# Performance work log

Hardware: AMD Instinct MI355X
Metric: run time of the kernel (lower is better)

## Reference

```python
import jax, jax.numpy as jnp
import numpy as np

EPS = 1e-5  # BatchNorm eps (PyTorch default)


def gcn_conv(x, edge_index, W, b):
    """PyG GCNConv with add_self_loops=True, normalize=True.
    out[j] = sum_{(i->j)} x_w[i] / sqrt(deg_i * deg_j) + x_w[j] / deg_j + b,
    deg_j = 1 + in-degree(j) (self-loop included)."""
    n = x.shape[0]
    src, dst = edge_index[0], edge_index[1]
    ones = jnp.ones(src.shape[0], x.dtype)
    deg = 1.0 + jax.ops.segment_sum(ones, dst, num_segments=n)  # [n]
    dis = jax.lax.rsqrt(deg)
    xw = x @ W  # [n, out]
    msg = xw[src] * (dis[src] * dis[dst])[:, None]  # gather + per-edge norm
    agg = jax.ops.segment_sum(msg, dst, num_segments=n)  # scatter-add
    agg = agg + xw * (1.0 / deg)[:, None]  # self-loop term
    return agg + b


def bn_relu(x, gamma, beta):
    # BatchNorm1d over the node dim (training-mode batch stats) + ReLU
    mean = x.mean(axis=0)
    var = x.var(axis=0)
    return jax.nn.relu((x - mean) * jax.lax.rsqrt(var + EPS) * gamma + beta)


def wireframe_gnn(x, edge_index, layers, fcW, fcb):
    feats = [x]
    h = x
    for (W, b, g, be) in layers:  # fixed small n_layers loop
        h = bn_relu(gcn_conv(h, edge_index, W, b), g, be)
        feats.append(h)
    cat = jnp.concatenate(feats, axis=1)
    return jax.nn.relu(cat @ fcW + fcb)


N_L, N_J = 50000, 25000
D_FC, NF = 1024, 256
E_L, E_J = 400000, 100000
L_LAB, J_LAB = 10, 3


def setup_inputs() -> dict:
    key = jax.random.key(0)
    ks = iter(jax.random.split(key, 48))
    p = lambda shape: (jax.random.normal(next(ks), shape, jnp.float32) * 0.02)
    inp = {}
    inp["line_features"] = jax.random.normal(next(ks), (N_L, D_FC), jnp.float32)
    inp["junction_features"] = jax.random.normal(next(ks), (N_J, NF), jnp.float32)
    inp["line_edge_index"] = jax.random.randint(next(ks), (2, E_L), 0, N_L, jnp.int64)
    inp["junction_edge_index"] = jax.random.randint(next(ks), (2, E_J), 0, N_J, jnp.int64)
    # line GNN: 1024 -> 512 -> 256, concat 1792 -> fc 1024
    inp["lg_W1"], inp["lg_b1"] = p((D_FC, D_FC // 2)), p((D_FC // 2,))
    inp["lg_g1"], inp["lg_be1"] = jnp.ones(D_FC // 2, jnp.float32), jnp.zeros(D_FC // 2, jnp.float32)
    inp["lg_W2"], inp["lg_b2"] = p((D_FC // 2, D_FC // 4)), p((D_FC // 4,))
    inp["lg_g2"], inp["lg_be2"] = jnp.ones(D_FC // 4, jnp.float32), jnp.zeros(D_FC // 4, jnp.float32)
    cat_l = D_FC + D_FC // 2 + D_FC // 4  # 1792
    inp["lg_fcW"], inp["lg_fcb"] = p((cat_l, D_FC)), p((D_FC,))
    # fc_lines: 1024 -> 1024 -> 1024 -> L_LAB (dim_loi*n_pts1 == dim_fc == 1024)
    inp["fl_W1"], inp["fl_b1"] = p((D_FC, D_FC)), p((D_FC,))
    inp["fl_W2"], inp["fl_b2"] = p((D_FC, D_FC)), p((D_FC,))
    inp["fl_W3"], inp["fl_b3"] = p((D_FC, L_LAB)), p((L_LAB,))
    # junction GNN: 256 -> 128 -> 64, concat 448 -> fc 256
    inp["jg_W1"], inp["jg_b1"] = p((NF, NF // 2)), p((NF // 2,))
    inp["jg_g1"], inp["jg_be1"] = jnp.ones(NF // 2, jnp.float32), jnp.zeros(NF // 2, jnp.float32)
    inp["jg_W2"], inp["jg_b2"] = p((NF // 2, NF // 4)), p((NF // 4,))
    inp["jg_g2"], inp["jg_be2"] = jnp.ones(NF // 4, jnp.float32), jnp.zeros(NF // 4, jnp.float32)
    cat_j = NF + NF // 2 + NF // 4  # 448
    inp["jg_fcW"], inp["jg_fcb"] = p((cat_j, NF)), p((NF,))
    # fc_junction: 256 -> 64 -> J_LAB
    m = NF // 4
    inp["fj_W1"], inp["fj_b1"] = p((NF, m)), p((m,))
    inp["fj_W2"], inp["fj_b2"] = p((m, J_LAB)), p((J_LAB,))
    return inp


def reference(line_features, junction_features, line_edge_index, junction_edge_index,
              lg_W1, lg_b1, lg_g1, lg_be1, lg_W2, lg_b2, lg_g2, lg_be2, lg_fcW, lg_fcb,
              fl_W1, fl_b1, fl_W2, fl_b2, fl_W3, fl_b3,
              jg_W1, jg_b1, jg_g1, jg_be1, jg_W2, jg_b2, jg_g2, jg_be2, jg_fcW, jg_fcb,
              fj_W1, fj_b1, fj_W2, fj_b2):
    # line branch
    h = wireframe_gnn(line_features, line_edge_index,
                      [(lg_W1, lg_b1, lg_g1, lg_be1), (lg_W2, lg_b2, lg_g2, lg_be2)],
                      lg_fcW, lg_fcb)
    h = jax.nn.relu(h @ fl_W1 + fl_b1)
    h = jax.nn.relu(h @ fl_W2 + fl_b2)
    line_logits = h @ fl_W3 + fl_b3
    # junction branch
    g = wireframe_gnn(junction_features, junction_edge_index,
                      [(jg_W1, jg_b1, jg_g1, jg_be1), (jg_W2, jg_b2, jg_g2, jg_be2)],
                      jg_fcW, jg_fcb)
    g = jax.nn.relu(g @ fj_W1 + fj_b1)
    junction_logits = g @ fj_W2 + fj_b2
    return (line_logits, junction_logits)
```

## Files before the change

### kernel.cpp

```cpp
#include <hip/hip_runtime.h>
#include <stdint.h>
#include <stddef.h>

typedef _Float16 f16;
typedef _Float16 f16x8 __attribute__((ext_vector_type(8)));
typedef _Float16 f16x4_t __attribute__((ext_vector_type(4)));
typedef float floatx4 __attribute__((ext_vector_type(4)));

template <int N> struct F16Vec { typedef f16 type __attribute__((ext_vector_type(N))); };

#define BN_EPS 1e-5f

struct WtJob { const float* W; f16* Wt; int K; int N; int tN; int tilebase; };
struct WtBatch { WtJob j[12]; int njobs; int ntiles; };

__global__ void k_wt_tiled(WtBatch b) {
  __shared__ float T[32][33];
  int bt = blockIdx.x;
  int i = 0;
  #pragma unroll 1
  while (i + 1 < b.njobs && bt >= b.j[i + 1].tilebase) ++i;
  WtJob J = b.j[i];
  int t = bt - J.tilebase;
  int tr = t / J.tN, tc = t - tr * J.tN;
  int ty = threadIdx.x >> 5, tx = threadIdx.x & 31;
  #pragma unroll
  for (int s = 0; s < 32; s += 8) {
    int k = tr * 32 + ty + s, n = tc * 32 + tx;
    if (k < J.K && n < J.N) T[ty + s][tx] = J.W[(size_t)k * J.N + n];
  }
  __syncthreads();
  #pragma unroll
  for (int s = 0; s < 32; s += 8) {
    int n = tc * 32 + ty + s, k = tr * 32 + tx;
    if (n < J.N && k < J.K) J.Wt[(size_t)n * J.K + k] = (f16)T[tx][ty + s];
  }
}

__global__ void k_cvt_cols(const float* __restrict__ src, f16* __restrict__ dst,
                           int n, int c, int ldd, int coff) {
  int t = blockIdx.x * blockDim.x + threadIdx.x;
  int cq = c >> 2;
  if (t >= n * cq) return;
  int r = t / cq, j = (t - r * cq) << 2;
  float4 v = *(const float4*)(src + (size_t)r * c + j);
  f16x4_t o; o[0] = (f16)v.x; o[1] = (f16)v.y; o[2] = (f16)v.z; o[3] = (f16)v.w;
  *(f16x4_t*)(dst + (size_t)r * ldd + coff + j) = o;
}

__global__ void k_count2(const int* __restrict__ dL, int EL, int* __restrict__ cntL,
                         const int* __restrict__ dJ, int EJ, int* __restrict__ cntJ) {
  int t = blockIdx.x * blockDim.x + threadIdx.x;
  if (t < EL) atomicAdd(&cntL[dL[t]], 1);
  else if (t < EL + EJ) atomicAdd(&cntJ[dJ[t - EL]], 1);
}

__global__ void k_scan4(const int* __restrict__ cnt, int n, int* __restrict__ rowstart,
                        float* __restrict__ dis) {
  __shared__ int wsum[16];
  __shared__ int carry_s;
  int tid = threadIdx.x, lane = tid & 63, wv = tid >> 6;
  if (tid == 0) { carry_s = 0; rowstart[0] = 0; }
  __syncthreads();
  for (int base = 0; base < n; base += 4096) {
    int i4 = base + tid * 4;
    int4 c = {0, 0, 0, 0};
    if (i4 < n) c = *(const int4*)(cnt + i4);
    int s0 = c.x, s1 = s0 + c.y, s2 = s1 + c.z, s3 = s2 + c.w;
    int x = s3;
    #pragma unroll
    for (int off = 1; off < 64; off <<= 1) {
      int y = __shfl_up(x, off, 64);
      if (lane >= off) x += y;
    }
    if (lane == 63) wsum[wv] = x;
    __syncthreads();
    if (wv == 0) {
      int s = (lane < 16) ? wsum[lane] : 0;
      #pragma unroll
      for (int off = 1; off < 16; off <<= 1) {
        int y = __shfl_up(s, off, 64);
        if (lane >= off) s += y;
      }
      if (lane < 16) wsum[lane] = s;
    }
    __syncthreads();
    int waveoff = (wv == 0) ? 0 : wsum[wv - 1];
    int excl = (x - s3) + waveoff + carry_s;
    if (i4 < n) {
      rowstart[i4 + 1] = excl + s0;
      rowstart[i4 + 2] = excl + s1;
      rowstart[i4 + 3] = excl + s2;
      rowstart[i4 + 4] = excl + s3;
      dis[i4 + 0] = rsqrtf(1.0f + (float)c.x);
      dis[i4 + 1] = rsqrtf(1.0f + (float)c.y);
      dis[i4 + 2] = rsqrtf(1.0f + (float)c.z);
      dis[i4 + 3] = rsqrtf(1.0f + (float)c.w);
    }
    __syncthreads();
    if (tid == 1023) carry_s = excl + s3;
    __syncthreads();
  }
}

__global__ void k_fill2(const int* __restrict__ eiL, int EL, const int* __restrict__ rsL,
                        int* __restrict__ fillL, int* __restrict__ cixL,
                        const int* __restrict__ eiJ, int EJ, const int* __restrict__ rsJ,
                        int* __restrict__ fillJ, int* __restrict__ cixJ) {
  int t = blockIdx.x * blockDim.x + threadIdx.x;
  if (t < EL) {
    int s = eiL[t], d = eiL[EL + t];
    int pos = atomicAdd(&fillL[d], 1);
    cixL[rsL[d] + pos] = s;
  } else if (t < EL + EJ) {
    int u = t - EL;
    int s = eiJ[u], d = eiJ[EJ + u];
    int pos = atomicAdd(&fillJ[d], 1);
    cixJ[rsJ[d] + pos] = s;
  }
}

template <int CPL>
__global__ void k_gather_f16(const f16* __restrict__ xw, int C,
                             const int* __restrict__ rowstart, const int* __restrict__ colidx,
                             const float* __restrict__ dis, const float* __restrict__ bias,
                             f16* __restrict__ dst, int ldd, int coff, int n) {
  typedef typename F16Vec<CPL>::type V;
  int w = threadIdx.x >> 6, l = threadIdx.x & 63;
  int j = blockIdx.x * 4 + w;
  if (j >= n) return;
  float dj = dis[j];
  int rs = rowstart[j], re = rowstart[j + 1];
  int c0 = l * CPL;
  float acc[CPL];
  {
    V p = *(const V*)(xw + (size_t)j * C + c0);
    float s = dj * dj;
    #pragma unroll
    for (int t = 0; t < CPL; ++t) acc[t] = (float)p[t] * s;
  }
  int e = rs;
  for (; e + 2 <= re; e += 2) {
    int s0 = colidx[e], s1 = colidx[e + 1];
    float f0 = dis[s0] * dj, f1 = dis[s1] * dj;
    V p0 = *(const V*)(xw + (size_t)s0 * C + c0);
    V p1 = *(const V*)(xw + (size_t)s1 * C + c0);
    #pragma unroll
    for (int t = 0; t < CPL; ++t) acc[t] += (float)p0[t] * f0 + (float)p1[t] * f1;
  }
  if (e < re) {
    int s0 = colidx[e];
    float f0 = dis[s0] * dj;
    V p0 = *(const V*)(xw + (size_t)s0 * C + c0);
    #pragma unroll
    for (int t = 0; t < CPL; ++t) acc[t] += (float)p0[t] * f0;
  }
  V o;
  #pragma unroll
  for (int t = 0; t < CPL; ++t) o[t] = (f16)(acc[t] + bias[c0 + t]);
  *(V*)(dst + (size_t)j * ldd + coff + c0) = o;
}

__global__ void k_stats(const f16* __restrict__ v, int ldd, int coff, int n, int C,
                        float* __restrict__ sum, float* __restrict__ sumsq) {
  int c = blockIdx.x * blockDim.x + threadIdx.x;
  if (c >= C) return;
  int r0 = blockIdx.y * 128, r1 = min(r0 + 128, n);
  float s = 0.f, s2 = 0.f;
  for (int r = r0; r < r1; ++r) {
    float x = (float)v[(size_t)r * ldd + coff + c];
    s += x; s2 += x * x;
  }
  atomicAdd(&sum[c], s);
  atomicAdd(&sumsq[c], s2);
}

__global__ void k_bnparam(const float* __restrict__ sum, const float* __restrict__ sumsq,
                          const float* __restrict__ gamma, const float* __restrict__ beta,
                          int n, int C, float* __restrict__ scale, float* __restrict__ shift) {
  int c = blockIdx.x * blockDim.x + threadIdx.x;
  if (c >= C) return;
  float mean = sum[c] / (float)n;
  float var = sumsq[c] / (float)n - mean * mean;
  float sc = gamma[c] * rsqrtf(var + BN_EPS);
  scale[c] = sc;
  shift[c] = beta[c] - mean * sc;
}

__global__ void k_bnapply_ip(f16* __restrict__ v, int ldd, int coff, int n, int C,
                             const float* __restrict__ scale, const float* __restrict__ shift) {
  int t = blockIdx.x * blockDim.x + threadIdx.x;
  int cq = C >> 2;
  if (t >= n * cq) return;
  int r = t / cq, c = (t - r * cq) << 2;
  f16* p = v + (size_t)r * ldd + coff + c;
  f16x4_t x = *(f16x4_t*)p;
  float4 sc = *(const float4*)(scale + c);
  float4 sh = *(const float4*)(shift + c);
  f16x4_t o;
  o[0] = (f16)fmaxf((float)x[0] * sc.x + sh.x, 0.f);
  o[1] = (f16)fmaxf((float)x[1] * sc.y + sh.y, 0.f);
  o[2] = (f16)fmaxf((float)x[2] * sc.z + sh.z, 0.f);
  o[3] = (f16)fmaxf((float)x[3] * sc.w + sh.w, 0.f);
  *(f16x4_t*)p = o;
}

__global__ __launch_bounds__(256)
void k_gemm(const f16* __restrict__ A, int lda,
            const f16* __restrict__ Bt,
            void* __restrict__ Cv, int ldc,
            const float* __restrict__ bias, int relu, int outf,
            int M, int N, int K, int mt, int nt, int per) {
  __shared__ f16 Ash[2][128 * 32];
  __shared__ f16 Bsh[2][128 * 32];
  int b = blockIdx.x;
  int g = (b & 7) * per + (b >> 3);
  if (g >= mt * nt) return;
  int tm = (g / nt) * 128, tn = (g % nt) * 128;
  int tid = threadIdx.x, l = tid & 63, w = tid >> 6;

  const f16* ag[2]; const f16* bg[2];
  uint32_t lof[2];
  #pragma unroll
  for (int j = 0; j < 2; ++j) {
    int rl = w * 32 + j * 16 + (l >> 2);
    int ck = l & 3;
    int lc = ck ^ ((rl >> 1) & 3);
    int gr = tm + rl; if (gr > M - 1) gr = M - 1;
    int gn = tn + rl; if (gn > N - 1) gn = N - 1;
    ag[j] = A + (size_t)gr * lda + lc * 8;
    bg[j] = Bt + (size_t)gn * K + lc * 8;
    lof[j] = (uint32_t)(w * 32 + j * 16) * 64;
  }

  int wm = (w >> 1) * 64, wn = (w & 1) * 64;
  int q = l >> 4, l15 = l & 15;
  uint32_t aoffb[4], boffb[4];
  #pragma unroll
  for (int i = 0; i < 4; ++i) {
    int m = wm + i * 16 + l15;
    int n2 = wn + i * 16 + l15;
    aoffb[i] = (uint32_t)(m * 32 + (q ^ ((m >> 1) & 3)) * 8) * 2;
    boffb[i] = (uint32_t)(n2 * 32 + (q ^ ((n2 >> 1) & 3)) * 8) * 2;
  }

  floatx4 acc[4][4];
  #pragma unroll
  for (int i = 0; i < 4; ++i)
    #pragma unroll
    for (int j = 0; j < 4; ++j) acc[i][j] = (floatx4){0.f, 0.f, 0.f, 0.f};

  int nk = K >> 5;
  #pragma unroll
  for (int j = 0; j < 2; ++j) {
    __builtin_amdgcn_global_load_lds(
        (const __attribute__((address_space(1))) void*)ag[j],
        (__attribute__((address_space(3))) void*)((char*)Ash + lof[j]), 16, 0, 0);
    __builtin_amdgcn_global_load_lds(
        (const __attribute__((address_space(1))) void*)bg[j],
        (__attribute__((address_space(3))) void*)((char*)Bsh + lof[j]), 16, 0, 0);
    ag[j] += 32; bg[j] += 32;
  }

  for (int i = 0; i < nk; ++i) {
    __syncthreads();
    if (i + 1 < nk) {
      uint32_t d = ((i + 1) & 1) ? 8192u : 0u;
      #pragma unroll
      for (int j = 0; j < 2; ++j) {
        __builtin_amdgcn_global_load_lds(
            (const __attribute__((address_space(1))) void*)ag[j],
            (__attribute__((address_space(3))) void*)((char*)Ash + d + lof[j]), 16, 0, 0);
        __builtin_amdgcn_global_load_lds(
            (const __attribute__((address_space(1))) void*)bg[j],
            (__attribute__((address_space(3))) void*)((char*)Bsh + d + lof[j]), 16, 0, 0);
        ag[j] += 32; bg[j] += 32;
      }
    }
    uint32_t s = (i & 1) ? 8192u : 0u;
    f16x8 af[4], bf[4];
    #pragma unroll
    for (int ii = 0; ii < 4; ++ii) {
      af[ii] = *(const f16x8*)((const char*)Ash + s + aoffb[ii]);
      bf[ii] = *(const f16x8*)((const char*)Bsh + s + boffb[ii]);
    }
    #pragma unroll
    for (int mi = 0; mi < 4; ++mi)
      #pragma unroll
      for (int ni = 0; ni < 4; ++ni)
        acc[mi][ni] = __builtin_amdgcn_mfma_f32_16x16x32_f16(af[mi], bf[ni], acc[mi][ni], 0, 0, 0);
  }

  #pragma unroll
  for (int ni = 0; ni < 4; ++ni) {
    int col = tn + wn + ni * 16 + l15;
    if (col >= N) continue;
    float bv = bias ? bias[col] : 0.f;
    #pragma unroll
    for (int mi = 0; mi < 4; ++mi) {
      int rowb = tm + wm + mi * 16 + q * 4;
      #pragma unroll
      for (int r = 0; r < 4; ++r) {
        int row = rowb + r;
        if (row < M) {
          float v = acc[mi][ni][r] + bv;
          if (relu) v = fmaxf(v, 0.f);
          if (outf) ((float*)Cv)[(size_t)row * ldc + col] = v;
          else      ((f16*)Cv)[(size_t)row * ldc + col] = (f16)v;
        }
      }
    }
  }
}

#define G_BAR()   __builtin_amdgcn_s_barrier()
#define G_LGKM0() asm volatile("s_waitcnt lgkmcnt(0)" ::: "memory")

#define READ_BF_ALL()                                                         \
  _Pragma("unroll")                                                           \
  for (int ni = 0; ni < 4; ++ni) {                                            \
    bf[ni][0] = *(const f16x8*)(cbp + bbase + ni * 2048 + cof0);              \
    bf[ni][1] = *(const f16x8*)(cbp + bbase + ni * 2048 + cof1);              \
  }

#define READ_AFP(DST, P)                                                      \
  DST[0] = *(const f16x8*)(cbp + abase + (2 * (P)) * 2048 + cof0);            \
  DST[1] = *(const f16x8*)(cbp + abase + (2 * (P)) * 2048 + cof1);            \
  DST[2] = *(const f16x8*)(cbp + abase + (2 * (P) + 1) * 2048 + cof0);        \
  DST[3] = *(const f16x8*)(cbp + abase + (2 * (P) + 1) * 2048 + cof1);

#define MFMA_PAIR(SRC, P)                                                     \
  _Pragma("unroll")                                                           \
  for (int ni = 0; ni < 4; ++ni) {                                            \
    acc[2*(P)][ni]   = __builtin_amdgcn_mfma_f32_16x16x32_f16(bf[ni][0], SRC[0], acc[2*(P)][ni], 0, 0, 0);   \
    acc[2*(P)+1][ni] = __builtin_amdgcn_mfma_f32_16x16x32_f16(bf[ni][0], SRC[2], acc[2*(P)+1][ni], 0, 0, 0); \
    acc[2*(P)][ni]   = __builtin_amdgcn_mfma_f32_16x16x32_f16(bf[ni][1], SRC[1], acc[2*(P)][ni], 0, 0, 0);   \
    acc[2*(P)+1][ni] = __builtin_amdgcn_mfma_f32_16x16x32_f16(bf[ni][1], SRC[3], acc[2*(P)+1][ni], 0, 0, 0); \
  }

__global__ __launch_bounds__(512, 2)
void k_gemm256(const f16* __restrict__ A, int lda,
               const f16* __restrict__ Bt,
               f16* __restrict__ C, int ldc,
               const float* __restrict__ bias, int relu,
               int M, int N, int K, int mt, int nt) {
  __shared__ char lds[131072];
  char* ldsc = (char*)lds;
  int nwg = mt * nt;
  int b = blockIdx.x;
  int xcd = b & 7, lid = b >> 3;
  int q8 = nwg >> 3, r8 = nwg & 7;
  int wg = (xcd < r8 ? xcd * (q8 + 1) : r8 * (q8 + 1) + (xcd - r8) * q8) + lid;
  int tm = (wg / nt) * 256, tn = (wg % nt) * 256;
  int tid = threadIdx.x, l = tid & 63, w = tid >> 6;
  int wm = w >> 2, wn = w & 3;
  int q = l >> 4, l15 = l & 15;
  int nk = K >> 6;

  int r0 = tid >> 3, r1 = r0 + 64;
  int ck = (tid & 7) ^ (r0 & 7);
  int gmA0a = tm + r0;        if (gmA0a > M - 1) gmA0a = M - 1;
  int gmA0b = tm + r1;        if (gmA0b > M - 1) gmA0b = M - 1;
  int gmA1a = tm + 128 + r0;  if (gmA1a > M - 1) gmA1a = M - 1;
  int gmA1b = tm + 128 + r1;  if (gmA1b > M - 1) gmA1b = M - 1;
  int gnB0a = tn + r0;        if (gnB0a > N - 1) gnB0a = N - 1;
  int gnB0b = tn + r1;        if (gnB0b > N - 1) gnB0b = N - 1;
  int gnB1a = tn + 128 + r0;  if (gnB1a > N - 1) gnB1a = N - 1;
  int gnB1b = tn + 128 + r1;  if (gnB1b > N - 1) gnB1b = N - 1;
  const f16* pA0a = A + (size_t)gmA0a * lda + ck * 8;
  const f16* pA0b = A + (size_t)gmA0b * lda + ck * 8;
  const f16* pA1a = A + (size_t)gmA1a * lda + ck * 8;
  const f16* pA1b = A + (size_t)gmA1b * lda + ck * 8;
  const f16* pB0a = Bt + (size_t)gnB0a * K + ck * 8;
  const f16* pB0b = Bt + (size_t)gnB0b * K + ck * 8;
  const f16* pB1a = Bt + (size_t)gnB1a * K + ck * 8;
  const f16* pB1b = Bt + (size_t)gnB1b * K + ck * 8;
  uint32_t dst0 = (uint32_t)tid * 16;

  auto ST2 = [&](const f16*& pa, const f16*& pb, uint32_t dst) {
    __builtin_amdgcn_global_load_lds(
        (const __attribute__((address_space(1))) void*)pa,
        (__attribute__((address_space(3))) void*)(ldsc + dst), 16, 0, 0);
    __builtin_amdgcn_global_load_lds(
        (const __attribute__((address_space(1))) void*)pb,
        (__attribute__((address_space(3))) void*)(ldsc + dst + 8192), 16, 0, 0);
    pa += 64; pb += 64;
  };
  auto SA0 = [&](uint32_t bb) { ST2(pA0a, pA0b, bb + dst0); };
  auto SA1 = [&](uint32_t bb) { ST2(pA1a, pA1b, bb + 16384u + dst0); };
  auto SB0 = [&](uint32_t bb) { ST2(pB0a, pB0b, bb + 32768u + dst0); };
  auto SB1 = [&](uint32_t bb) { ST2(pB1a, pB1b, bb + 49152u + dst0); };

  uint32_t abase = (uint32_t)((wm * 128 + l15) * 128);
  uint32_t bbase = (uint32_t)(32768 + (wn * 64 + l15) * 128);
  uint32_t cof0 = (uint32_t)(((0 + q) ^ (l15 & 7)) * 16);
  uint32_t cof1 = (uint32_t)(((4 + q) ^ (l15 & 7)) * 16);

  floatx4 acc[8][4];
  #pragma unroll
  for (int i = 0; i < 8; ++i)
    #pragma unroll
    for (int j = 0; j < 4; ++j) acc[i][j] = (floatx4){0.f, 0.f, 0.f, 0.f};

  SA0(0u); SA1(0u); SB0(0u); SB1(0u);
  if (nk > 1) { SB0(65536u); SB1(65536u); }

  f16x8 bf[4][2], af0[4], af1[4], af2[4], af3[4];
  for (int t = 0; t < nk; ++t) {
    uint32_t cb = (t & 1) ? 65536u : 0u;
    uint32_t ob = 65536u - cb;
    const char* cbp = ldsc + cb;
    if (t + 1 < nk) { asm volatile("s_waitcnt vmcnt(4)" ::: "memory"); }
    else            { asm volatile("s_waitcnt vmcnt(0)" ::: "memory"); }
    G_BAR();
    __builtin_amdgcn_sched_barrier(0);
    if (t + 1 < nk) { SA0(ob); SA1(ob); }
    READ_BF_ALL();
    READ_AFP(af0, 0);
    READ_AFP(af1, 1);
    MFMA_PAIR(af0, 0);
    G_LGKM0();
    G_BAR();
    if (t + 2 < nk) { SB0(cb); SB1(cb); }
    READ_AFP(af2, 2);
    MFMA_PAIR(af1, 1);
    READ_AFP(af3, 3);
    MFMA_PAIR(af2, 2);
    MFMA_PAIR(af3, 3);
  }

  #pragma unroll
  for (int mi = 0; mi < 8; ++mi) {
    int m = tm + wm * 128 + mi * 16 + l15;
    if (m >= M) continue;
    f16* crow = C + (size_t)m * ldc;
    #pragma unroll
    for (int ni = 0; ni < 4; ++ni) {
      int n0 = tn + wn * 64 + ni * 16 + q * 4;
      floatx4 v = acc[mi][ni];
      if (bias) {
        float4 bv = *(const float4*)(bias + n0);
        v[0] += bv.x; v[1] += bv.y; v[2] += bv.z; v[3] += bv.w;
      }
      if (relu) {
        v[0] = fmaxf(v[0], 0.f); v[1] = fmaxf(v[1], 0.f);
        v[2] = fmaxf(v[2], 0.f); v[3] = fmaxf(v[3], 0.f);
      }
      f16x4_t o;
      o[0] = (f16)v[0]; o[1] = (f16)v[1]; o[2] = (f16)v[2]; o[3] = (f16)v[3];
      *(f16x4_t*)(crow + n0) = o;
    }
  }
}

extern "C" void kernel_launch(void* const* d_in, const int* in_sizes, int n_in,
                              void* d_out, int out_size, void* d_ws, size_t ws_size,
                              hipStream_t stream) {
  (void)in_sizes; (void)n_in; (void)out_size; (void)ws_size;
  const int NL = 50000, NJ = 25000, EL = 400000, EJ = 100000;

  const float* x_l  = (const float*)d_in[0];
  const float* x_j  = (const float*)d_in[1];
  const int*   ei_l = (const int*)d_in[2];
  const int*   ei_j = (const int*)d_in[3];
  const float* lgW1 = (const float*)d_in[4];  const float* lgb1 = (const float*)d_in[5];
  const float* lgg1 = (const float*)d_in[6];  const float* lgbe1= (const float*)d_in[7];
  const float* lgW2 = (const float*)d_in[8];  const float* lgb2 = (const float*)d_in[9];
  const float* lgg2 = (const float*)d_in[10]; const float* lgbe2= (const float*)d_in[11];
  const float* lgfcW= (const float*)d_in[12]; const float* lgfcb= (const float*)d_in[13];
  const float* flW1 = (const float*)d_in[14]; const float* flb1 = (const float*)d_in[15];
  const float* flW2 = (const float*)d_in[16]; const float* flb2 = (const float*)d_in[17];
  const float* flW3 = (const float*)d_in[18]; const float* flb3 = (const float*)d_in[19];
  const float* jgW1 = (const float*)d_in[20]; const float* jgb1 = (const float*)d_in[21];
  const float* jgg1 = (const float*)d_in[22]; const float* jgbe1= (const float*)d_in[23];
  const float* jgW2 = (const float*)d_in[24]; const float* jgb2 = (const float*)d_in[25];
  const float* jgg2 = (const float*)d_in[26]; const float* jgbe2= (const float*)d_in[27];
  const float* jgfcW= (const float*)d_in[28]; const float* jgfcb= (const float*)d_in[29];
  const float* fjW1 = (const float*)d_in[30]; const float* fjb1 = (const float*)d_in[31];
  const float* fjW2 = (const float*)d_in[32]; const float* fjb2 = (const float*)d_in[33];

  char* ws = (char*)d_ws;
  size_t off = 0;
  auto alloc = [&](size_t bytes) -> char* {
    char* p = ws + off;
    off += (bytes + 255) & ~(size_t)255;
    return p;
  };

  f16* cat16 = (f16*)alloc((size_t)NL * 1792 * 2);
  f16* hA    = (f16*)alloc((size_t)NL * 1024 * 2);
  f16* hB    = (f16*)alloc((size_t)NL * 1024 * 2);
  f16*  xw16  = (f16*)hB;
  f16* catJ  = (f16*)alloc((size_t)NJ * 448 * 2);
  f16* hJA   = (f16*)alloc((size_t)NJ * 256 * 2);
  f16* hJB   = (f16*)alloc((size_t)NJ * 64 * 2);
  f16*  xwJ   = (f16*)hB;

  f16* W1t   = (f16*)alloc((size_t)1024 * 512 * 2);
  f16* W2t   = (f16*)alloc((size_t)512 * 256 * 2);
  f16* fcWt  = (f16*)alloc((size_t)1792 * 1024 * 2);
  f16* flW1t = (f16*)alloc((size_t)1024 * 1024 * 2);
  f16* flW2t = (f16*)alloc((size_t)1024 * 1024 * 2);
  f16* flW3t = (f16*)alloc((size_t)1024 * 16 * 2);
  f16* jW1t  = (f16*)alloc((size_t)256 * 128 * 2);
  f16* jW2t  = (f16*)alloc((size_t)128 * 64 * 2);
  f16* jfcWt = (f16*)alloc((size_t)448 * 256 * 2);
  f16* fjW1t = (f16*)alloc((size_t)256 * 64 * 2);
  f16* fjW2t = (f16*)alloc((size_t)64 * 4 * 2);

  int* zero0 = (int*)alloc(((size_t)2 * NL + 2 * NJ + 1920) * 4);
  int* cntL  = zero0;
  int* fillL = cntL + NL;
  int* cntJ  = fillL + NL;
  int* fillJ = cntJ + NJ;
  float* stats = (float*)(fillJ + NJ);
  float* sum1L = stats;        float* sq1L = stats + 512;
  float* sum2L = stats + 1024; float* sq2L = stats + 1280;
  float* sum1J = stats + 1536; float* sq1J = stats + 1664;
  float* sum2J = stats + 1792; float* sq2J = stats + 1856;

  int* rsL   = (int*)alloc((size_t)(NL + 4) * 4);
  int* cixL  = (int*)alloc((size_t)EL * 4);
  float* disL= (float*)alloc((size_t)NL * 4);
  int* rsJ   = (int*)alloc((size_t)(NJ + 4) * 4);
  int* cixJ  = (int*)alloc((size_t)EJ * 4);
  float* disJ= (float*)alloc((size_t)NJ * 4);
  float* scalc = (float*)alloc(512 * 4);
  float* shftc = (float*)alloc(512 * 4);

  auto cdiv = [](int a, int b) { return (a + b - 1) / b; };

  auto gemm = [&](const f16* A, int lda, const f16* Bt, void* Cc, int ldc,
                  const float* bias, int relu, int outf, int M, int N, int K) {
    if (!outf && (N & 255) == 0 && N >= 256 && (K & 63) == 0 && K >= 128) {
      int mt = cdiv(M, 256), nt = N >> 8;
      k_gemm256<<<mt * nt, 512, 0, stream>>>(A, lda, Bt, (f16*)Cc, ldc, bias, relu,
                                             M, N, K, mt, nt);
    } else {
      int mt = cdiv(M, 128), nt = cdiv(N, 128);
      int per = cdiv(mt * nt, 8);
      k_gemm<<<8 * per, 256, 0, stream>>>(A, lda, Bt, Cc, ldc, bias, relu, outf,
                                          M, N, K, mt, nt, per);
    }
  };
  auto bn = [&](f16* v, int ldd, int coff, int n, int C,
                float* sum, float* sumsq, const float* gamma, const float* beta) {
    dim3 gs(cdiv(C, 256), cdiv(n, 128));
    k_stats<<<gs, 256, 0, stream>>>(v, ldd, coff, n, C, sum, sumsq);
    k_bnparam<<<cdiv(C, 256), 256, 0, stream>>>(sum, sumsq, gamma, beta, n, C, scalc, shftc);
    k_bnapply_ip<<<cdiv(n * (C >> 2), 256), 256, 0, stream>>>(v, ldd, coff, n, C, scalc, shftc);
  };

  hipMemsetAsync(zero0, 0, ((size_t)2 * NL + 2 * NJ + 1920) * 4, stream);

  {
    WtBatch B2; int base = 0, nj = 0;
    auto add = [&](const float* W, f16* Wt, int K, int N) {
      int tK = cdiv(K, 32), tN = cdiv(N, 32);
      B2.j[nj++] = WtJob{W, Wt, K, N, tN, base};
      base += tK * tN;
    };
    add(lgW1, W1t, 1024, 512);
    add(lgW2, W2t, 512, 256);
    add(lgfcW, fcWt, 1792, 1024);
    add(flW1, flW1t, 1024, 1024);
    add(flW2, flW2t, 1024, 1024);
    add(flW3, flW3t, 1024, 10);
    add(jgW1, jW1t, 256, 128);
    add(jgW2, jW2t, 128, 64);
    add(jgfcW, jfcWt, 448, 256);
    add(fjW1, fjW1t, 256, 64);
    add(fjW2, fjW2t, 64, 3);
    B2.njobs = nj; B2.ntiles = base;
    k_wt_tiled<<<base, 256, 0, stream>>>(B2);
  }

  k_cvt_cols<<<cdiv(NL * 256, 256), 256, 0, stream>>>(x_l, cat16, NL, 1024, 1792, 0);
  k_cvt_cols<<<cdiv(NJ * 64, 256), 256, 0, stream>>>(x_j, catJ, NJ, 256, 448, 0);

  k_count2<<<cdiv(EL + EJ, 256), 256, 0, stream>>>(ei_l + EL, EL, cntL, ei_j + EJ, EJ, cntJ);
  k_scan4<<<1, 1024, 0, stream>>>(cntL, NL, rsL, disL);
  k_scan4<<<1, 1024, 0, stream>>>(cntJ, NJ, rsJ, disJ);
  k_fill2<<<cdiv(EL + EJ, 256), 256, 0, stream>>>(ei_l, EL, rsL, fillL, cixL,
                                                  ei_j, EJ, rsJ, fillJ, cixJ);

  gemm(cat16, 1792, W1t, xw16, 512, nullptr, 0, 0, NL, 512, 1024);
  k_gather_f16<8><<<cdiv(NL, 4), 256, 0, stream>>>(xw16, 512, rsL, cixL, disL, lgb1,
                                                   cat16, 1792, 1024, NL);
  bn(cat16, 1792, 1024, NL, 512, sum1L, sq1L, lgg1, lgbe1);

  gemm(cat16 + 1024, 1792, W2t, xw16, 256, nullptr, 0, 0, NL, 256, 512);
  k_gather_f16<4><<<cdiv(NL, 4), 256, 0, stream>>>(xw16, 256, rsL, cixL, disL, lgb2,
                                                   cat16, 1792, 1536, NL);
  bn(cat16, 1792, 1536, NL, 256, sum2L, sq2L, lgg2, lgbe2);

  gemm(cat16, 1792, fcWt, hA, 1024, lgfcb, 1, 0, NL, 1024, 1792);
  gemm(hA, 1024, flW1t, hB, 1024, flb1, 1, 0, NL, 1024, 1024);
  gemm(hB, 1024, flW2t, hA, 1024, flb2, 1, 0, NL, 1024, 1024);
  gemm(hA, 1024, flW3t, (float*)d_out, 10, flb3, 0, 1, NL, 10, 1024);

  gemm(catJ, 448, jW1t, xwJ, 128, nullptr, 0, 0, NJ, 128, 256);
  k_gather_f16<2><<<cdiv(NJ, 4), 256, 0, stream>>>(xwJ, 128, rsJ, cixJ, disJ, jgb1,
                                                   catJ, 448, 256, NJ);
  bn(catJ, 448, 256, NJ, 128, sum1J, sq1J, jgg1, jgbe1);

  gemm(catJ + 256, 448, jW2t, xwJ, 64, nullptr, 0, 0, NJ, 64, 128);
  k_gather_f16<1><<<cdiv(NJ, 4), 256, 0, stream>>>(xwJ, 64, rsJ, cixJ, disJ, jgb2,
                                                   catJ, 448, 384, NJ);
  bn(catJ, 448, 384, NJ, 64, sum2J, sq2J, jgg2, jgbe2);

  gemm(catJ, 448, jfcWt, hJA, 256, jgfcb, 1, 0, NJ, 256, 448);
  gemm(hJA, 256, fjW1t, hJB, 64, fjb1, 1, 0, NJ, 64, 256);
  gemm(hJB, 64, fjW2t, (float*)d_out + (size_t)NL * 10, 3, fjb2, 0, 1, NJ, 3, 64);
}
```

Baseline: 1.449 ms.

## Load GEMM B fragments directly from global memory instead of staging through LDS

The 256x256 GEMM kernel no longer stages the transposed weight tile (B) in shared memory. Each wave now reads its B fragments straight from global memory into registers, which halves the LDS footprint and drops the mid-iteration barrier and lgkm wait. The cost is that every k-step waits on vmcnt(0), so the A prefetch no longer overlaps as deeply. B rows are also re-read by each wave row group rather than shared, and the B row clamp for partial N tiles is gone.

```diff
diff --git a/kernel.cpp b/kernel.cpp
--- a/kernel.cpp
+++ b/kernel.cpp
@@ -314,14 +314,6 @@
 }
 
 #define G_BAR()   __builtin_amdgcn_s_barrier()
-#define G_LGKM0() asm volatile("s_waitcnt lgkmcnt(0)" ::: "memory")
-
-#define READ_BF_ALL()                                                         \
-  _Pragma("unroll")                                                           \
-  for (int ni = 0; ni < 4; ++ni) {                                            \
-    bf[ni][0] = *(const f16x8*)(cbp + bbase + ni * 2048 + cof0);              \
-    bf[ni][1] = *(const f16x8*)(cbp + bbase + ni * 2048 + cof1);              \
-  }
 
 #define READ_AFP(DST, P)                                                      \
   DST[0] = *(const f16x8*)(cbp + abase + (2 * (P)) * 2048 + cof0);            \
@@ -344,7 +336,7 @@
                f16* __restrict__ C, int ldc,
                const float* __restrict__ bias, int relu,
                int M, int N, int K, int mt, int nt) {
-  __shared__ char lds[131072];
+  __shared__ char lds[65536];
   char* ldsc = (char*)lds;
   int nwg = mt * nt;
   int b = blockIdx.x;
@@ -363,18 +355,10 @@
   int gmA0b = tm + r1;        if (gmA0b > M - 1) gmA0b = M - 1;
   int gmA1a = tm + 128 + r0;  if (gmA1a > M - 1) gmA1a = M - 1;
   int gmA1b = tm + 128 + r1;  if (gmA1b > M - 1) gmA1b = M - 1;
-  int gnB0a = tn + r0;        if (gnB0a > N - 1) gnB0a = N - 1;
-  int gnB0b = tn + r1;        if (gnB0b > N - 1) gnB0b = N - 1;
-  int gnB1a = tn + 128 + r0;  if (gnB1a > N - 1) gnB1a = N - 1;
-  int gnB1b = tn + 128 + r1;  if (gnB1b > N - 1) gnB1b = N - 1;
   const f16* pA0a = A + (size_t)gmA0a * lda + ck * 8;
   const f16* pA0b = A + (size_t)gmA0b * lda + ck * 8;
   const f16* pA1a = A + (size_t)gmA1a * lda + ck * 8;
   const f16* pA1b = A + (size_t)gmA1b * lda + ck * 8;
-  const f16* pB0a = Bt + (size_t)gnB0a * K + ck * 8;
-  const f16* pB0b = Bt + (size_t)gnB0b * K + ck * 8;
-  const f16* pB1a = Bt + (size_t)gnB1a * K + ck * 8;
-  const f16* pB1b = Bt + (size_t)gnB1b * K + ck * 8;
   uint32_t dst0 = (uint32_t)tid * 16;
 
   auto ST2 = [&](const f16*& pa, const f16*& pb, uint32_t dst) {
@@ -388,11 +372,11 @@
   };
   auto SA0 = [&](uint32_t bb) { ST2(pA0a, pA0b, bb + dst0); };
   auto SA1 = [&](uint32_t bb) { ST2(pA1a, pA1b, bb + 16384u + dst0); };
-  auto SB0 = [&](uint32_t bb) { ST2(pB0a, pB0b, bb + 32768u + dst0); };
-  auto SB1 = [&](uint32_t bb) { ST2(pB1a, pB1b, bb + 49152u + dst0); };
+
+  const f16* pB = Bt + (size_t)(tn + wn * 64 + l15) * K + q * 8;
+  size_t r16 = (size_t)16 * K;
 
   uint32_t abase = (uint32_t)((wm * 128 + l15) * 128);
-  uint32_t bbase = (uint32_t)(32768 + (wn * 64 + l15) * 128);
   uint32_t cof0 = (uint32_t)(((0 + q) ^ (l15 & 7)) * 16);
   uint32_t cof1 = (uint32_t)(((4 + q) ^ (l15 & 7)) * 16);
 
@@ -402,26 +386,27 @@
     #pragma unroll
     for (int j = 0; j < 4; ++j) acc[i][j] = (floatx4){0.f, 0.f, 0.f, 0.f};
 
-  SA0(0u); SA1(0u); SB0(0u); SB1(0u);
-  if (nk > 1) { SB0(65536u); SB1(65536u); }
+  SA0(0u); SA1(0u);
 
   f16x8 bf[4][2], af0[4], af1[4], af2[4], af3[4];
   for (int t = 0; t < nk; ++t) {
-    uint32_t cb = (t & 1) ? 65536u : 0u;
-    uint32_t ob = 65536u - cb;
+    uint32_t cb = (t & 1) ? 32768u : 0u;
+    uint32_t ob = 32768u - cb;
     const char* cbp = ldsc + cb;
-    if (t + 1 < nk) { asm volatile("s_waitcnt vmcnt(4)" ::: "memory"); }
-    else            { asm volatile("s_waitcnt vmcnt(0)" ::: "memory"); }
+    asm volatile("s_waitcnt vmcnt(0)" ::: "memory");
     G_BAR();
     __builtin_amdgcn_sched_barrier(0);
+    #pragma unroll
+    for (int ni = 0; ni < 4; ++ni) {
+      bf[ni][0] = *(const f16x8*)(pB + ni * r16);
+      bf[ni][1] = *(const f16x8*)(pB + ni * r16 + 32);
+    }
+    pB += 64;
+    __builtin_amdgcn_sched_barrier(0x38F);
     if (t + 1 < nk) { SA0(ob); SA1(ob); }
-    READ_BF_ALL();
     READ_AFP(af0, 0);
     READ_AFP(af1, 1);
     MFMA_PAIR(af0, 0);
-    G_LGKM0();
-    G_BAR();
-    if (t + 2 < nk) { SB0(cb); SB1(cb); }
     READ_AFP(af2, 2);
     MFMA_PAIR(af1, 1);
     READ_AFP(af3, 3);
```

After: 1.844 ms. 27.2% more time.
